# Kernel optimization log

Hardware: AMD Instinct MI355X
Metric: run time of the kernel (lower is better)

The kernel has to match this reference:

```python
import jax, jax.numpy as jnp
import numpy as np

N_NODES = 100000
N_EDGES = 3200000
K_STEPS = 10
ALPHA = 0.1


def setup_inputs() -> dict:
    key = jax.random.key(0)
    k1, k2, k3, k4 = jax.random.split(key, 4)
    x = jax.random.normal(k1, (N_NODES, 512), dtype=jnp.float32)
    edge_index = jax.random.randint(k2, (2, N_EDGES), 0, N_NODES, dtype=jnp.int32)
    # Glorot-ish scaled params for lin1/lin2
    W1 = jax.random.normal(k3, (512, 256), dtype=jnp.float32) * (1.0 / np.sqrt(512))
    b1 = jnp.zeros((256,), dtype=jnp.float32)
    W2 = jax.random.normal(k4, (256, 64), dtype=jnp.float32) * (1.0 / np.sqrt(256))
    b2 = jnp.zeros((64,), dtype=jnp.float32)
    return {"x": x, "edge_index": edge_index, "W1": W1, "b1": b1, "W2": W2, "b2": b2}


def _gcn_norm(edge_index, num_nodes):
    # Add self-loops, compute symmetric normalization coefficients (PyG gcn_norm).
    loop = jnp.arange(num_nodes, dtype=edge_index.dtype)
    row = jnp.concatenate([edge_index[0], loop])
    col = jnp.concatenate([edge_index[1], loop])
    deg = jax.ops.segment_sum(jnp.ones_like(col, dtype=jnp.float32), col,
                              num_segments=num_nodes)
    dinv = jnp.where(deg > 0, jax.lax.rsqrt(deg), 0.0)
    norm = dinv[row] * dinv[col]  # [E + N]
    return row, col, norm


def reference(x, edge_index, W1, b1, W2, b2):
    # Inference mode: dropout is identity (training=False).
    h = jax.nn.relu(x @ W1 + b1) @ W2 + b2  # [N, out]
    num_nodes = x.shape[0]
    row, col, norm = _gcn_norm(edge_index, num_nodes)

    def step(z, _):
        msg = norm[:, None] * z[row]  # gather + scale, [E+N, out]
        agg = jax.ops.segment_sum(msg, col, num_segments=num_nodes)
        return (1.0 - ALPHA) * agg + ALPHA * h, None

    z, _ = jax.lax.scan(step, h, None, length=K_STEPS)
    return jax.nn.log_softmax(z, axis=1)
```

## Files before the change

### kernel.cpp

```cpp
#include <hip/hip_runtime.h>
#include <hip/hip_bf16.h>

typedef __attribute__((ext_vector_type(8))) short   short8;
typedef __attribute__((ext_vector_type(4))) short   shortx4;
typedef __attribute__((ext_vector_type(8))) __bf16  bf16x8;
typedef __attribute__((ext_vector_type(4))) float   floatx4;

__device__ inline float bf2f(short u) {
    return __builtin_bit_cast(float, (unsigned)((unsigned short)u) << 16);
}
__device__ inline short f2bf(float f) {
    return __builtin_bit_cast(short, __float2bfloat16(f));
}

__device__ inline void gll16(const void* g, void* l) {
    __builtin_amdgcn_global_load_lds(
        (const __attribute__((address_space(1))) unsigned int*)g,
        (__attribute__((address_space(3))) unsigned int*)l, 16, 0, 0);
}


__global__ void count_kernel(const int* __restrict__ col, int* __restrict__ icnt, int E) {
    int e = blockIdx.x * 256 + threadIdx.x;
    if (e < E) atomicAdd(&icnt[col[e]], 1);
}

__global__ void dinv_cursor_kernel(const int* __restrict__ icnt, float* __restrict__ dinv,
                                   int* __restrict__ cursor, int N) {
    int i = blockIdx.x * 256 + threadIdx.x;
    if (i < N) { dinv[i] = rsqrtf((float)(icnt[i] + 1)); cursor[i] = 0; }
}


__global__ __launch_bounds__(256) void blocksum_kernel(const int* __restrict__ icnt,
                                                       int* __restrict__ bsum, int N) {
    int b = blockIdx.x, t = threadIdx.x;
    int base = b * 1024 + t * 4;
    int s = 0;
    if (base + 3 < N) {
        int4 v = *(const int4*)&icnt[base];
        s = v.x + v.y + v.z + v.w;
    } else {
        for (int i = 0; i < 4; i++) if (base + i < N) s += icnt[base + i];
    }
    __shared__ int red[256];
    red[t] = s;
    __syncthreads();
    for (int o = 128; o > 0; o >>= 1) {
        if (t < o) red[t] += red[t + o];
        __syncthreads();
    }
    if (t == 0) bsum[b] = red[0];
}

__global__ __launch_bounds__(128) void bscan_kernel(int* __restrict__ bsum,
                                                    int* __restrict__ offs, int NB, int N) {
    __shared__ int sh[128];
    int t = threadIdx.x;
    int v = (t < NB) ? bsum[t] : 0;
    sh[t] = v;
    __syncthreads();
    for (int o = 1; o < 128; o <<= 1) {
        int u = (t >= o) ? sh[t - o] : 0;
        __syncthreads();
        sh[t] += u;
        __syncthreads();
    }
    if (t < NB) bsum[t] = sh[t] - v;
    if (t == 127) offs[N] = sh[127];
}

__global__ __launch_bounds__(256) void offs_kernel(const int* __restrict__ icnt,
                                                   const int* __restrict__ bsum,
                                                   int* __restrict__ offs, int N) {
    int b = blockIdx.x, t = threadIdx.x;
    int base = b * 1024 + t * 4;
    int v[4]; int s = 0;
#pragma unroll
    for (int i = 0; i < 4; i++) {
        int idx = base + i;
        v[i] = (idx < N) ? icnt[idx] : 0;
        s += v[i];
    }
    __shared__ int sh[256];
    sh[t] = s;
    __syncthreads();
    for (int o = 1; o < 256; o <<= 1) {
        int u = (t >= o) ? sh[t - o] : 0;
        __syncthreads();
        sh[t] += u;
        __syncthreads();
    }
    int off = bsum[b] + sh[t] - s;
#pragma unroll
    for (int i = 0; i < 4; i++) {
        int idx = base + i;
        if (idx < N) { offs[idx] = off; off += v[i]; }
    }
}


__global__ void w1_tile_kernel(const float* __restrict__ src,
                               __hip_bfloat16* __restrict__ dst) {
    int t = blockIdx.x * 256 + threadIdx.x;
    if (t < 512 * 256) {
        int k = t >> 8, n = t & 255;
        int kc = k >> 5, kl = k & 31;
        int slot = kl >> 3, pos = kl & 7;
        int sl = slot ^ ((n >> 1) & 3);
        dst[kc * 8192 + n * 32 + sl * 8 + pos] = __float2bfloat16(src[t]);
    }
}

__global__ void transpose_cvt_kernel(const float* __restrict__ src,
                                     __hip_bfloat16* __restrict__ dst, int K, int N) {
    int t = blockIdx.x * 256 + threadIdx.x;
    if (t < K * N) { int k = t / N, n = t % N; dst[n * K + k] = __float2bfloat16(src[t]); }
}


__global__ __launch_bounds__(256) void mlp_scatter_kernel(
    const float* __restrict__ x, const __hip_bfloat16* __restrict__ W1Tt,
    const float* __restrict__ b1, const __hip_bfloat16* __restrict__ W2T,
    const float* __restrict__ b2, __hip_bfloat16* __restrict__ h, int M, int MB,
    const int* __restrict__ row, const int* __restrict__ col,
    const int* __restrict__ offs, int* __restrict__ cursor,
    int* __restrict__ csr, int E)
{
    __shared__ __align__(16) short lds[16384];
    short* Ts = lds;

    if (blockIdx.x >= MB) {
        int e = (blockIdx.x - MB) * 256 + threadIdx.x;
        if (e < E) {
            int c = col[e];
            int p = offs[c] + atomicAdd(&cursor[c], 1);
            csr[p] = row[e];
        }
        return;
    }

    const int t = threadIdx.x;
    const int lane = t & 63, wave = t >> 6;
    const int lm = lane & 15, quad = lane >> 4;
    const int block_m = blockIdx.x * 64;
    const short* w2s = (const short*)W2T;
    const char*  w1b = (const char*)W1Tt;

    const int grow = block_m + wave * 16 + lm;
    const bool rok = grow < M;
    const float* xrow = x + (size_t)grow * 512 + quad * 8;
    const floatx4 z4 = (floatx4){0.f, 0.f, 0.f, 0.f};

    const int chunk_base = wave * 4;
    const int gl_off = lane * 16;

    auto stageB = [&](int kc, int buf) {
#pragma unroll
        for (int it = 0; it < 4; it++) {
            int chunk = chunk_base + it;
            gll16(w1b + (size_t)kc * 16384 + chunk * 1024 + gl_off,
                  &lds[buf * 8192 + chunk * 512]);
        }
    };

    floatx4 accA[16];
#pragma unroll
    for (int i = 0; i < 16; i++) accA[i] = z4;

    stageB(0, 0);
    floatx4 a0  = rok ? *(const floatx4*)xrow       : z4;
    floatx4 a1  = rok ? *(const floatx4*)(xrow + 4) : z4;
    floatx4 na0 = z4, na1 = z4;

    const int boff = lm * 32 + ((quad ^ ((lm >> 1) & 3)) << 3);

    __syncthreads();

    for (int kc = 0; kc < 16; kc++) {
        if (kc < 15) {
            stageB(kc + 1, (kc + 1) & 1);
            const float* p = xrow + (kc + 1) * 32;
            na0 = rok ? *(const floatx4*)p       : z4;
            na1 = rok ? *(const floatx4*)(p + 4) : z4;
        }
        short8 afs;
#pragma unroll
        for (int j = 0; j < 4; j++) { afs[j] = f2bf(a0[j]); afs[4 + j] = f2bf(a1[j]); }
        bf16x8 af = __builtin_bit_cast(bf16x8, afs);
        const short* bb = &lds[(kc & 1) * 8192];
#pragma unroll
        for (int nt = 0; nt < 16; nt++) {
            bf16x8 bfr = __builtin_bit_cast(bf16x8, *(const short8*)&bb[nt * 512 + boff]);
            accA[nt] = __builtin_amdgcn_mfma_f32_16x16x32_bf16(af, bfr, accA[nt], 0, 0, 0);
        }
        a0 = na0; a1 = na1;
        __syncthreads();
    }

    floatx4 accB[4];
#pragma unroll
    for (int j = 0; j < 4; j++) accB[j] = z4;

#pragma unroll
    for (int s = 0; s < 4; s++) {
        __syncthreads();
#pragma unroll
        for (int ntl = 0; ntl < 4; ntl++) {
            int nt = s * 4 + ntl;
            float bv = b1[nt * 16 + lm];
#pragma unroll
            for (int r = 0; r < 4; r++) {
                int rowl = wave * 16 + quad * 4 + r;
                Ts[rowl * 72 + ntl * 16 + lm] = f2bf(fmaxf(accA[nt][r] + bv, 0.f));
            }
        }
        __syncthreads();
#pragma unroll
        for (int kk = 0; kk < 2; kk++) {
            bf16x8 af2 = __builtin_bit_cast(bf16x8,
                *(const short8*)&Ts[(wave * 16 + lm) * 72 + kk * 32 + quad * 8]);
#pragma unroll
            for (int nt = 0; nt < 4; nt++) {
                bf16x8 bfr = __builtin_bit_cast(bf16x8,
                    *(const short8*)&w2s[(size_t)(nt * 16 + lm) * 256 + s * 64 + kk * 32 + quad * 8]);
                accB[nt] = __builtin_amdgcn_mfma_f32_16x16x32_bf16(af2, bfr, accB[nt], 0, 0, 0);
            }
        }
    }

#pragma unroll
    for (int nt = 0; nt < 4; nt++) {
        int colg = nt * 16 + lm;
        float bv = b2[colg];
#pragma unroll
        for (int r = 0; r < 4; r++) {
            int rowg = block_m + wave * 16 + quad * 4 + r;
            if (rowg < M)
                h[(size_t)rowg * 64 + colg] = __float2bfloat16(accB[nt][r] + bv);
        }
    }
}


__global__ __launch_bounds__(256) void prop_kernel(
    const __hip_bfloat16* __restrict__ z_in, const __hip_bfloat16* __restrict__ h,
    const float* __restrict__ dinv, const int* __restrict__ offs,
    const int* __restrict__ csr, __hip_bfloat16* __restrict__ z_out,
    float* __restrict__ out, int N, int last)
{
    int node = blockIdx.x * 4 + (threadIdx.x >> 6);
    if (node >= N) return;
    int lane = threadIdx.x & 63;
    int g = lane >> 3, i = lane & 7;
    const short* zs = (const short*)z_in;
    const short* hs = (const short*)h;
    float di = dinv[node];
    int s = offs[node], e = offs[node + 1];
    float acc[8] = {0.f, 0.f, 0.f, 0.f, 0.f, 0.f, 0.f, 0.f};

    for (int j0 = s; j0 < e; j0 += 64) {
        int jj = j0 + lane;
        int nbr = 0; float dn = 0.f;
        if (jj < e) { nbr = csr[jj]; dn = dinv[nbr]; }
        int cnt = min(64, e - j0);
        bool more = cnt > 32;

        int nb[8]; float wv[8];
#pragma unroll
        for (int tt = 0; tt < 8; tt++) {
            int src = tt * 8 + g;
            nb[tt] = __shfl(nbr, src);
            wv[tt] = __shfl(dn, src);
        }

        short8 zv[8];
#pragma unroll
        for (int tt = 0; tt < 4; tt++)
            zv[tt] = *(const short8*)&zs[(size_t)nb[tt] * 64 + i * 8];
        if (more) {
#pragma unroll
            for (int tt = 4; tt < 8; tt++)
                zv[tt] = *(const short8*)&zs[(size_t)nb[tt] * 64 + i * 8];
        }
#pragma unroll
        for (int tt = 0; tt < 4; tt++)
#pragma unroll
            for (int j = 0; j < 8; j++)
                acc[j] = fmaf(wv[tt], bf2f(zv[tt][j]), acc[j]);
        if (more) {
#pragma unroll
            for (int tt = 4; tt < 8; tt++)
#pragma unroll
                for (int j = 0; j < 8; j++)
                    acc[j] = fmaf(wv[tt], bf2f(zv[tt][j]), acc[j]);
        }
    }
#pragma unroll
    for (int j = 0; j < 8; j++) {
        acc[j] += __shfl_xor(acc[j], 8);
        acc[j] += __shfl_xor(acc[j], 16);
        acc[j] += __shfl_xor(acc[j], 32);
    }

    short8 zv = *(const short8*)&zs[(size_t)node * 64 + i * 8];
    short8 hv = *(const short8*)&hs[(size_t)node * 64 + i * 8];
    float v[8];
#pragma unroll
    for (int j = 0; j < 8; j++)
        v[j] = 0.9f * (di * acc[j] + di * di * bf2f(zv[j])) + 0.1f * bf2f(hv[j]);

    if (!last) {
        if (g == 0) {
            short8 o8;
#pragma unroll
            for (int j = 0; j < 8; j++) o8[j] = f2bf(v[j]);
            *(short8*)&((short*)z_out)[(size_t)node * 64 + i * 8] = o8;
        }
    } else {
        float m = v[0];
#pragma unroll
        for (int j = 1; j < 8; j++) m = fmaxf(m, v[j]);
        m = fmaxf(m, __shfl_xor(m, 1));
        m = fmaxf(m, __shfl_xor(m, 2));
        m = fmaxf(m, __shfl_xor(m, 4));
        float ss = 0.f;
#pragma unroll
        for (int j = 0; j < 8; j++) ss += expf(v[j] - m);
        ss += __shfl_xor(ss, 1);
        ss += __shfl_xor(ss, 2);
        ss += __shfl_xor(ss, 4);
        float ls = m + logf(ss);
        if (g == 0) {
            floatx4 o0, o1;
#pragma unroll
            for (int j = 0; j < 4; j++) { o0[j] = v[j] - ls; o1[j] = v[4 + j] - ls; }
            *(floatx4*)&out[(size_t)node * 64 + i * 8]     = o0;
            *(floatx4*)&out[(size_t)node * 64 + i * 8 + 4] = o1;
        }
    }
}


extern "C" void kernel_launch(void* const* d_in, const int* in_sizes, int n_in,
                              void* d_out, int out_size, void* d_ws, size_t ws_size,
                              hipStream_t stream) {
    const float* x  = (const float*)d_in[0];
    const int*   ei = (const int*)d_in[1];
    const float* W1 = (const float*)d_in[2];
    const float* b1 = (const float*)d_in[3];
    const float* W2 = (const float*)d_in[4];
    const float* b2 = (const float*)d_in[5];
    float* out = (float*)d_out;

    const int FIN = 512, FH = 256, FO = 64;
    const int N = in_sizes[0] / FIN;
    const int E = in_sizes[1] / 2;
    const int* erow = ei;
    const int* ecol = ei + E;

    char* w = (char*)d_ws;
    size_t o = 0;
    auto take = [&](size_t bytes) -> void* {
        void* p = w + o;
        o += (bytes + 511) & ~(size_t)511;
        return p;
    };
    int*   icnt   = (int*)  take((size_t)N * 4);
    float* dinv   = (float*)take((size_t)N * 4);
    int*   offs   = (int*)  take((size_t)(N + 1) * 4);
    int*   cursor = (int*)  take((size_t)N * 4);
    int*   csr    = (int*)  take((size_t)E * 4);
    int*   bsum   = (int*)  take((size_t)128 * 4);
    __hip_bfloat16* W1Tt = (__hip_bfloat16*)take((size_t)FIN * FH * 2);
    __hip_bfloat16* W2T  = (__hip_bfloat16*)take((size_t)FH * FO * 2);
    __hip_bfloat16* hbuf = (__hip_bfloat16*)take((size_t)N * FO * 2);
    __hip_bfloat16* zA   = (__hip_bfloat16*)take((size_t)N * FO * 2);
    __hip_bfloat16* zB   = (__hip_bfloat16*)out;

    const int NB = (N + 1023) / 1024;

    (void)hipMemsetAsync(icnt, 0, (size_t)N * 4, stream);
    count_kernel<<<(E + 255) / 256, 256, 0, stream>>>(ecol, icnt, E);
    dinv_cursor_kernel<<<(N + 255) / 256, 256, 0, stream>>>(icnt, dinv, cursor, N);
    blocksum_kernel<<<NB, 256, 0, stream>>>(icnt, bsum, N);
    bscan_kernel<<<1, 128, 0, stream>>>(bsum, offs, NB, N);
    offs_kernel<<<NB, 256, 0, stream>>>(icnt, bsum, offs, N);
    w1_tile_kernel<<<(FIN * FH + 255) / 256, 256, 0, stream>>>(W1, W1Tt);
    transpose_cvt_kernel<<<(FH * FO + 255) / 256, 256, 0, stream>>>(W2, W2T, FH, FO);

    const int MB = (N + 63) / 64;
    const int SB = (E + 255) / 256;
    mlp_scatter_kernel<<<MB + SB, 256, 0, stream>>>(x, W1Tt, b1, W2T, b2, hbuf, N, MB,
                                                    erow, ecol, offs, cursor, csr, E);

    const __hip_bfloat16* zin = hbuf;
    for (int k = 0; k < 10; k++) {
        int last = (k == 9);
        __hip_bfloat16* zout = (k & 1) ? zB : zA;
        prop_kernel<<<(N + 3) / 4, 256, 0, stream>>>(zin, hbuf, dinv, offs, csr,
                                                     zout, out, N, last);
        zin = zout;
    }
}
```

Measured before the change: 1.213 ms.

## Pack neighbor dinv into CSR and interleave MLP with scatter blocks

The CSR array now stores (neighbor index, dinv[neighbor]) pairs, filled in during the scatter phase. Each propagation step then reads the weight directly instead of doing a dependent random gather into dinv. The fused MLP/scatter launch also interleaves MLP blocks among scatter blocks (every R-th block) so compute-heavy and atomic-heavy work run together instead of back to back. The cost is that CSR traffic doubles to 8 bytes per edge in every propagation step.

```diff
diff --git a/kernel.cpp b/kernel.cpp
--- a/kernel.cpp
+++ b/kernel.cpp
@@ -122,20 +122,27 @@
 __global__ __launch_bounds__(256) void mlp_scatter_kernel(
     const float* __restrict__ x, const __hip_bfloat16* __restrict__ W1Tt,
     const float* __restrict__ b1, const __hip_bfloat16* __restrict__ W2T,
-    const float* __restrict__ b2, __hip_bfloat16* __restrict__ h, int M, int MB,
+    const float* __restrict__ b2, __hip_bfloat16* __restrict__ h, int M, int MB, int R,
     const int* __restrict__ row, const int* __restrict__ col,
     const int* __restrict__ offs, int* __restrict__ cursor,
-    int* __restrict__ csr, int E)
+    int* __restrict__ csrw, const float* __restrict__ dinv, int E)
 {
     __shared__ __align__(16) short lds[16384];
     short* Ts = lds;
 
-    if (blockIdx.x >= MB) {
-        int e = (blockIdx.x - MB) * 256 + threadIdx.x;
+    const int bid = blockIdx.x;
+    const int mid = bid / R;
+    const bool isMlp = (bid % R == 0) && (mid < MB);
+
+    if (!isMlp) {
+        int sIdx = bid - min((bid + R - 1) / R, MB);
+        int e = sIdx * 256 + threadIdx.x;
         if (e < E) {
             int c = col[e];
+            int r = row[e];
+            float wv = dinv[r];
             int p = offs[c] + atomicAdd(&cursor[c], 1);
-            csr[p] = row[e];
+            *(int2*)&csrw[(size_t)p * 2] = make_int2(r, __float_as_int(wv));
         }
         return;
     }
@@ -143,7 +150,7 @@
     const int t = threadIdx.x;
     const int lane = t & 63, wave = t >> 6;
     const int lm = lane & 15, quad = lane >> 4;
-    const int block_m = blockIdx.x * 64;
+    const int block_m = mid * 64;
     const short* w2s = (const short*)W2T;
     const char*  w1b = (const char*)W1Tt;
 
@@ -246,7 +253,7 @@
 __global__ __launch_bounds__(256) void prop_kernel(
     const __hip_bfloat16* __restrict__ z_in, const __hip_bfloat16* __restrict__ h,
     const float* __restrict__ dinv, const int* __restrict__ offs,
-    const int* __restrict__ csr, __hip_bfloat16* __restrict__ z_out,
+    const int* __restrict__ csrw, __hip_bfloat16* __restrict__ z_out,
     float* __restrict__ out, int N, int last)
 {
     int node = blockIdx.x * 4 + (threadIdx.x >> 6);
@@ -255,6 +262,7 @@
     int g = lane >> 3, i = lane & 7;
     const short* zs = (const short*)z_in;
     const short* hs = (const short*)h;
+    const int2* cw = (const int2*)csrw;
     float di = dinv[node];
     int s = offs[node], e = offs[node + 1];
     float acc[8] = {0.f, 0.f, 0.f, 0.f, 0.f, 0.f, 0.f, 0.f};
@@ -262,7 +270,7 @@
     for (int j0 = s; j0 < e; j0 += 64) {
         int jj = j0 + lane;
         int nbr = 0; float dn = 0.f;
-        if (jj < e) { nbr = csr[jj]; dn = dinv[nbr]; }
+        if (jj < e) { int2 v2 = cw[jj]; nbr = v2.x; dn = __int_as_float(v2.y); }
         int cnt = min(64, e - j0);
         bool more = cnt > 32;
 
@@ -370,7 +378,7 @@
     float* dinv   = (float*)take((size_t)N * 4);
     int*   offs   = (int*)  take((size_t)(N + 1) * 4);
     int*   cursor = (int*)  take((size_t)N * 4);
-    int*   csr    = (int*)  take((size_t)E * 4);
+    int*   csrw   = (int*)  take((size_t)E * 8);
     int*   bsum   = (int*)  take((size_t)128 * 4);
     __hip_bfloat16* W1Tt = (__hip_bfloat16*)take((size_t)FIN * FH * 2);
     __hip_bfloat16* W2T  = (__hip_bfloat16*)take((size_t)FH * FO * 2);
@@ -391,14 +399,16 @@
 
     const int MB = (N + 63) / 64;
     const int SB = (E + 255) / 256;
-    mlp_scatter_kernel<<<MB + SB, 256, 0, stream>>>(x, W1Tt, b1, W2T, b2, hbuf, N, MB,
-                                                    erow, ecol, offs, cursor, csr, E);
+    const int G  = MB + SB;
+    const int R  = G / MB;
+    mlp_scatter_kernel<<<G, 256, 0, stream>>>(x, W1Tt, b1, W2T, b2, hbuf, N, MB, R,
+                                              erow, ecol, offs, cursor, csrw, dinv, E);
 
     const __hip_bfloat16* zin = hbuf;
     for (int k = 0; k < 10; k++) {
         int last = (k == 9);
         __hip_bfloat16* zout = (k & 1) ? zB : zA;
-        prop_kernel<<<(N + 3) / 4, 256, 0, stream>>>(zin, hbuf, dinv, offs, csr,
+        prop_kernel<<<(N + 3) / 4, 256, 0, stream>>>(zin, hbuf, dinv, offs, csrw,
                                                      zout, out, N, last);
         zin = zout;
     }
```

Measured after the change: 1.745 ms. 43.9% more time.
